# Kernel tuning notes

Hardware: AMD Instinct MI355X
Metric: run time of the kernel (lower is better)

Reference implementation:

```python
import jax, jax.numpy as jnp
import numpy as np

# Faithful re-expression of the torch module:
#  - channel-mix einsum (64 -> 16)
#  - two sequential unfolds along the LAST spatial axis with kernel 3, pad 1
#    (the second unfold sees the zero-padding of the first as data, so padding
#    semantics compose: value at offset n+i+k-2 is zeroed if n+k-1 is out of
#    range OR n+i+k-2 is out of range)
#  - contraction against the [32,8,3,3] weight, reshape, and roll by +1 on H.
# shift_direction is random +/-1 in the original __init__; fixed to +1 here.

SHIFT = 1

def setup_inputs() -> dict:
    key = jax.random.key(0)
    k_x, k_w0, k_w1 = jax.random.split(key, 3)
    x = jax.random.normal(k_x, (1, 512, 14, 14), dtype=jnp.float32)
    w_conv = jax.random.normal(k_w0, (32, 8, 3, 3), dtype=jnp.float32)  # weights[0]
    w_mix = jax.random.normal(k_w1, (16, 64), dtype=jnp.float32)        # weights[1]
    return {"x": x, "w_conv": w_conv, "w_mix": w_mix}


def _unfold3_last(t):
    # emulate F.unfold with kernel (3,1), padding (1,0) along the last axis
    # t: (..., 14) -> (..., 3, 14), kernel-tap axis at -2 (matches torch layout)
    p = jnp.pad(t, [(0, 0)] * (t.ndim - 1) + [(1, 1)])
    return jnp.stack([p[..., i:i + 14] for i in range(3)], axis=-2)


def reference(x, w_conv, w_mix):
    t3 = x.reshape(1, 64, 8, 14, 14)
    # 'kjlmn, ij -> kilmn' : channel mix 64 -> 16
    t4 = jnp.einsum('kjlmn,ij->kilmn', t3, w_mix)           # (1,16,8,14,14)
    u1 = _unfold3_last(t4)                                   # (1,16,8,14,3,14)
    u2 = _unfold3_last(u1)                                   # (1,16,8,14,3,3,14) = mpjoikn
    t6 = jnp.einsum('mpjoikn,ljik->mlpon', u2, w_conv)       # (1,32,16,14,14)
    y = t6.reshape(1, 512, 14, 14)
    return jnp.roll(y, SHIFT, axis=2)
```

## Files before the change

### kernel.cpp

```cpp
#include <hip/hip_runtime.h>


__global__ __launch_bounds__(256) void fused_mix_unfold_conv(
    const float* __restrict__ x,
    const float* __restrict__ w_conv,
    const float* __restrict__ w_mix,
    float* __restrict__ out)
{
    const int o   = blockIdx.x;
    const int lh  = blockIdx.y;
    const int tid = threadIdx.x;

    __shared__ float sm_x[512 * 14];
    __shared__ float sm_t4[8 * 16 * 17];
    __shared__ float sm_wc[16 * 72];

    {
        const float2* x2  = (const float2*)x;
        float2* smx2 = (float2*)sm_x;
        #pragma unroll
        for (int i = 0; i < 14; ++i) {
            int idx = tid + i * 256;
            int ch = idx / 7, t7 = idx - ch * 7;
            smx2[idx] = x2[ch * 98 + o * 7 + t7];
        }
        for (int i = tid; i < 1152; i += 256)
            sm_wc[i] = w_conv[lh * 1152 + i];
    }
    __syncthreads();

    {
        const int wv   = tid >> 6;
        const int lane = tid & 63;
        const int pgrp = __builtin_amdgcn_readfirstlane(wv & 1);
        const int jn   = (wv >> 1) * 64 + lane;
        if (jn < 112) {
            const int j = jn / 14;
            const int n = jn - j * 14;
            float acc[8];
            #pragma unroll
            for (int pp = 0; pp < 8; ++pp) acc[pp] = 0.f;
            const float4* wm4 = (const float4*)(w_mix + pgrp * 512);
            #pragma unroll
            for (int q4 = 0; q4 < 16; ++q4) {
                float xv0 = sm_x[(q4 * 4 + 0) * 112 + jn];
                float xv1 = sm_x[(q4 * 4 + 1) * 112 + jn];
                float xv2 = sm_x[(q4 * 4 + 2) * 112 + jn];
                float xv3 = sm_x[(q4 * 4 + 3) * 112 + jn];
                #pragma unroll
                for (int pp = 0; pp < 8; ++pp) {
                    const float4 wq = wm4[pp * 16 + q4];
                    acc[pp] += xv0 * wq.x + xv1 * wq.y + xv2 * wq.z + xv3 * wq.w;
                }
            }
            #pragma unroll
            for (int pp = 0; pp < 8; ++pp)
                sm_t4[(j * 16 + pgrp * 8 + pp) * 17 + n] = acc[pp];
        }
    }
    __syncthreads();

    {
        const int p     = tid & 15;
        const int l_loc = tid >> 4;
        float acc[14];
        #pragma unroll
        for (int w = 0; w < 14; ++w) acc[w] = 0.f;

        #pragma unroll
        for (int j = 0; j < 8; ++j) {
            const float* row = &sm_t4[(j * 16 + p) * 17];
            float wt[9];
            #pragma unroll
            for (int t9 = 0; t9 < 9; ++t9)
                wt[t9] = sm_wc[l_loc * 72 + j * 9 + t9];
            #pragma unroll
            for (int w = 0; w < 14; ++w) {
                #pragma unroll
                for (int k1 = 0; k1 < 3; ++k1) {
                    #pragma unroll
                    for (int k2 = 0; k2 < 3; ++k2) {
                        const int n2 = w + k2 - 1;
                        const int ns = w + k1 + k2 - 2;
                        if (n2 >= 0 && n2 < 14 && ns >= 0 && ns < 14)
                            acc[w] += row[ns] * wt[k1 * 3 + k2];
                    }
                }
            }
        }

        const int h = (o == 13) ? 0 : (o + 1);
        const int c = lh * 256 + tid;
        float* op = out + c * 196 + h * 14;
        #pragma unroll
        for (int w = 0; w < 14; ++w) op[w] = acc[w];
    }
}

extern "C" void kernel_launch(void* const* d_in, const int* in_sizes, int n_in,
                              void* d_out, int out_size, void* d_ws, size_t ws_size,
                              hipStream_t stream) {
    const float* x      = (const float*)d_in[0];
    const float* w_conv = (const float*)d_in[1];
    const float* w_mix  = (const float*)d_in[2];
    float* out = (float*)d_out;
    dim3 grid(14, 2, 1);
    fused_mix_unfold_conv<<<grid, 256, 0, stream>>>(x, w_conv, w_mix, out);
}
```

Measured before the change: 67.04 us.

## Double grid, split channel-mix reduction across halves, and split conv width per thread

The grid goes from 28 to 56 blocks, each handling 8 output l-channels instead of 16. The 64-channel mix reduction is split across two thread halves, each reading x straight from global memory and writing partial sums to separate shared buffers. Those partials are summed when the conv stage loads its rows, and each thread computes 7 output columns instead of 14. The aim is more parallelism and less per-thread serial work on this tiny, latency-bound problem. The cost is that every block recomputes the full channel mix, and x is read from global memory without coalescing.

```diff
diff --git a/kernel.cpp b/kernel.cpp
--- a/kernel.cpp
+++ b/kernel.cpp
@@ -1,5 +1,44 @@
 #include <hip/hip_runtime.h>
 
+
+#define T4_STRIDE 17
+
+template <int WB>
+__device__ __forceinline__ void conv_half(const float (*t4)[8 * 16 * T4_STRIDE],
+                                          const float* __restrict__ wt,
+                                          int p, float* __restrict__ op) {
+    float acc[7];
+#pragma unroll
+    for (int w = 0; w < 7; ++w) acc[w] = 0.f;
+
+#pragma unroll
+    for (int j = 0; j < 8; ++j) {
+        const float* r0 = &t4[0][(j * 16 + p) * T4_STRIDE];
+        const float* r1 = &t4[1][(j * 16 + p) * T4_STRIDE];
+        float r[14];
+#pragma unroll
+        for (int n = 0; n < 14; ++n) r[n] = r0[n] + r1[n];
+        float w9[9];
+#pragma unroll
+        for (int t = 0; t < 9; ++t) w9[t] = wt[j * 9 + t];
+#pragma unroll
+        for (int w = 0; w < 7; ++w) {
+            const int ww = WB + w;
+#pragma unroll
+            for (int k1 = 0; k1 < 3; ++k1) {
+#pragma unroll
+                for (int k2 = 0; k2 < 3; ++k2) {
+                    const int n2 = ww + k2 - 1;
+                    const int ns = ww + k1 + k2 - 2;
+                    if (n2 >= 0 && n2 < 14 && ns >= 0 && ns < 14)
+                        acc[w] += r[ns] * w9[k1 * 3 + k2];
+                }
+            }
+        }
+    }
+#pragma unroll
+    for (int w = 0; w < 7; ++w) op[w] = acc[w];
+}
 
 __global__ __launch_bounds__(256) void fused_mix_unfold_conv(
     const float* __restrict__ x,
@@ -8,92 +47,58 @@
     float* __restrict__ out)
 {
     const int o   = blockIdx.x;
-    const int lh  = blockIdx.y;
+    const int lq  = blockIdx.y;
     const int tid = threadIdx.x;
 
-    __shared__ float sm_x[512 * 14];
-    __shared__ float sm_t4[8 * 16 * 17];
-    __shared__ float sm_wc[16 * 72];
+    __shared__ float sm_t4[2][8 * 16 * T4_STRIDE];
+    __shared__ float sm_wc[8 * 72];
+
+#pragma unroll
+    for (int i = tid; i < 576; i += 256) sm_wc[i] = w_conv[lq * 576 + i];
 
     {
-        const float2* x2  = (const float2*)x;
-        float2* smx2 = (float2*)sm_x;
-        #pragma unroll
-        for (int i = 0; i < 14; ++i) {
-            int idx = tid + i * 256;
-            int ch = idx / 7, t7 = idx - ch * 7;
-            smx2[idx] = x2[ch * 98 + o * 7 + t7];
-        }
-        for (int i = tid; i < 1152; i += 256)
-            sm_wc[i] = w_conv[lh * 1152 + i];
-    }
-    __syncthreads();
-
-    {
-        const int wv   = tid >> 6;
-        const int lane = tid & 63;
-        const int pgrp = __builtin_amdgcn_readfirstlane(wv & 1);
-        const int jn   = (wv >> 1) * 64 + lane;
+        const int qh = __builtin_amdgcn_readfirstlane(tid >> 7);
+        const int jn = tid & 127;
         if (jn < 112) {
             const int j = jn / 14;
             const int n = jn - j * 14;
-            float acc[8];
-            #pragma unroll
-            for (int pp = 0; pp < 8; ++pp) acc[pp] = 0.f;
-            const float4* wm4 = (const float4*)(w_mix + pgrp * 512);
-            #pragma unroll
-            for (int q4 = 0; q4 < 16; ++q4) {
-                float xv0 = sm_x[(q4 * 4 + 0) * 112 + jn];
-                float xv1 = sm_x[(q4 * 4 + 1) * 112 + jn];
-                float xv2 = sm_x[(q4 * 4 + 2) * 112 + jn];
-                float xv3 = sm_x[(q4 * 4 + 3) * 112 + jn];
-                #pragma unroll
-                for (int pp = 0; pp < 8; ++pp) {
-                    const float4 wq = wm4[pp * 16 + q4];
-                    acc[pp] += xv0 * wq.x + xv1 * wq.y + xv2 * wq.z + xv3 * wq.w;
+            float acc[16];
+#pragma unroll
+            for (int p = 0; p < 16; ++p) acc[p] = 0.f;
+
+            const float* xb = x + (qh * 32 * 8 + j) * 196 + o * 14 + n;
+            const float4* wm4 = (const float4*)w_mix + qh * 8;
+#pragma unroll
+            for (int q4 = 0; q4 < 8; ++q4) {
+                const float xv0 = xb[(q4 * 4 + 0) * 1568];
+                const float xv1 = xb[(q4 * 4 + 1) * 1568];
+                const float xv2 = xb[(q4 * 4 + 2) * 1568];
+                const float xv3 = xb[(q4 * 4 + 3) * 1568];
+#pragma unroll
+                for (int p = 0; p < 16; ++p) {
+                    const float4 wq = wm4[p * 16 + q4];
+                    acc[p] += xv0 * wq.x + xv1 * wq.y + xv2 * wq.z + xv3 * wq.w;
                 }
             }
-            #pragma unroll
-            for (int pp = 0; pp < 8; ++pp)
-                sm_t4[(j * 16 + pgrp * 8 + pp) * 17 + n] = acc[pp];
+#pragma unroll
+            for (int p = 0; p < 16; ++p)
+                sm_t4[qh][(j * 16 + p) * T4_STRIDE + n] = acc[p];
         }
     }
     __syncthreads();
 
     {
         const int p     = tid & 15;
-        const int l_loc = tid >> 4;
-        float acc[14];
-        #pragma unroll
-        for (int w = 0; w < 14; ++w) acc[w] = 0.f;
-
-        #pragma unroll
-        for (int j = 0; j < 8; ++j) {
-            const float* row = &sm_t4[(j * 16 + p) * 17];
-            float wt[9];
-            #pragma unroll
-            for (int t9 = 0; t9 < 9; ++t9)
-                wt[t9] = sm_wc[l_loc * 72 + j * 9 + t9];
-            #pragma unroll
-            for (int w = 0; w < 14; ++w) {
-                #pragma unroll
-                for (int k1 = 0; k1 < 3; ++k1) {
-                    #pragma unroll
-                    for (int k2 = 0; k2 < 3; ++k2) {
-                        const int n2 = w + k2 - 1;
-                        const int ns = w + k1 + k2 - 2;
-                        if (n2 >= 0 && n2 < 14 && ns >= 0 && ns < 14)
-                            acc[w] += row[ns] * wt[k1 * 3 + k2];
-                    }
-                }
-            }
-        }
-
-        const int h = (o == 13) ? 0 : (o + 1);
-        const int c = lh * 256 + tid;
+        const int l_loc = (tid >> 4) & 7;
+        const int wh    = __builtin_amdgcn_readfirstlane(tid >> 7);
+        const int h     = (o == 13) ? 0 : (o + 1);
+        const int c     = lq * 128 + (tid & 127);
+        const float* wt = sm_wc + l_loc * 72;
         float* op = out + c * 196 + h * 14;
-        #pragma unroll
-        for (int w = 0; w < 14; ++w) op[w] = acc[w];
+        if (wh == 0)
+            conv_half<0>(sm_t4, wt, p, op);
+        else
+            conv_half<7>(sm_t4, wt, p, op + 7);
     }
 }
 
@@ -104,6 +109,6 @@
     const float* w_conv = (const float*)d_in[1];
     const float* w_mix  = (const float*)d_in[2];
     float* out = (float*)d_out;
-    dim3 grid(14, 2, 1);
+    dim3 grid(14, 4, 1);
     fused_mix_unfold_conv<<<grid, 256, 0, stream>>>(x, w_conv, w_mix, out);
 }
```

Result: faster. 64.33 us (-4.0%).
